# Kernel tuning notes

Measured on AMD Instinct MI355X. Metric: run time of the kernel, lower is better.

Reference implementation:

```python
import jax, jax.numpy as jnp
import numpy as np

N, M, D = 8192, 8192, 256

def setup_inputs() -> dict:
    key = jax.random.key(0)
    kx, ky = jax.random.split(key)
    x = jax.random.normal(kx, (N, D), dtype=jnp.float32)
    y = jax.random.normal(ky, (M, D), dtype=jnp.float32)
    gamma = jnp.float32(1.0)  # learnable scalar parameter
    return {"x": x, "y": y, "gamma": gamma}

def reference(x, y, gamma):
    # Flatten trailing dims (matches x.view(x.size(0), -1))
    x = x.reshape(x.shape[0], -1)
    y = y.reshape(y.shape[0], -1)
    x_sq = jnp.sum(x * x, axis=-1)  # [N]
    y_sq = jnp.sum(y * y, axis=-1)  # [M]
    xy = x @ y.T                    # [N, M]
    sqdist = jnp.maximum(x_sq[:, None] + y_sq[None, :] - 2.0 * xy, 0.0)
    return jnp.exp(-gamma * sqdist)
```

## Files before the change

### kernel.cpp

```cpp
#include <hip/hip_runtime.h>
#include <stdint.h>


typedef __attribute__((ext_vector_type(4))) float f32x4;
typedef __attribute__((ext_vector_type(8))) int   i32x8;

#define NN 8192
#define MM 8192
#define DD 256
#define BK 128

__global__ __launch_bounds__(256) void prep_kernel(
    const float* __restrict__ x, const float* __restrict__ y,
    unsigned char* __restrict__ xb, unsigned char* __restrict__ yb,
    float* __restrict__ xsq, float* __restrict__ ysq) {
  const int lane = threadIdx.x & 63;
  const int row  = blockIdx.x * 4 + (threadIdx.x >> 6);

  const float* src = x;
  unsigned char* dst = xb;
  float* sq = xsq;
  int r = row;
  if (row >= NN) { src = y; dst = yb; sq = ysq; r = row - NN; }

  const float4 v = reinterpret_cast<const float4*>(src + (size_t)r * DD)[lane];
  float s = v.x * v.x + v.y * v.y + v.z * v.z + v.w * v.w;

  int w = 0;
  w = __builtin_amdgcn_cvt_pk_fp8_f32(v.x, v.y, w, false);
  w = __builtin_amdgcn_cvt_pk_fp8_f32(v.z, v.w, w, true);
  reinterpret_cast<int*>(dst + (size_t)r * DD)[lane] = w;

  #pragma unroll
  for (int o = 32; o > 0; o >>= 1) s += __shfl_down(s, o);
  if (lane == 0) sq[r] = s;
}

__global__ __launch_bounds__(256, 2) void rbf_gemm_kernel(
    const unsigned char* __restrict__ xb, const unsigned char* __restrict__ yb,
    const float* __restrict__ xsq, const float* __restrict__ ysq,
    const float* __restrict__ gamma, float* __restrict__ out) {
  __shared__ unsigned char As[128 * BK];
  __shared__ unsigned char Bs[128 * BK];

  const int tid   = threadIdx.x;
  const int lane  = tid & 63;
  const int wave  = tid >> 6;
  const int waveM = wave >> 1;
  const int waveN = wave & 1;
  const int row0  = blockIdx.y * 128;
  const int col0  = blockIdx.x * 128;

  f32x4 acc[4][4] = {};

  const int srow = lane >> 3;
  const int sseg = ((lane & 7) ^ (lane >> 3)) * 16;

  const int fm = lane & 15;
  const int g  = lane >> 4;
  const int off_lo = fm * 128 + (((2 * g)     ^ (fm & 7)) * 16);
  const int off_hi = fm * 128 + (((2 * g + 1) ^ (fm & 7)) * 16);

  #pragma unroll
  for (int kt = 0; kt < 2; ++kt) {
    const int kk = kt * BK;
    __syncthreads();
    #pragma unroll
    for (int q = 0; q < 2; ++q) {
      const int c = wave * 2 + q;
      #pragma unroll
      for (int p = 0; p < 2; ++p) {
        const unsigned char* ga =
            xb + (size_t)(row0 + c * 16 + p * 8 + srow) * DD + kk + sseg;
        __builtin_amdgcn_global_load_lds(
            (const __attribute__((address_space(1))) void*)ga,
            (__attribute__((address_space(3))) void*)(As + c * 2048 + p * 1024),
            16, 0, 0);
        const unsigned char* gb =
            yb + (size_t)(col0 + c * 16 + p * 8 + srow) * DD + kk + sseg;
        __builtin_amdgcn_global_load_lds(
            (const __attribute__((address_space(1))) void*)gb,
            (__attribute__((address_space(3))) void*)(Bs + c * 2048 + p * 1024),
            16, 0, 0);
      }
    }
    __syncthreads();

    i32x8 a[4], b[4];
    #pragma unroll
    for (int i = 0; i < 4; ++i) {
      const unsigned char* base = As + (waveM * 4 + i) * 2048;
      const int4 lo = *reinterpret_cast<const int4*>(base + off_lo);
      const int4 hi = *reinterpret_cast<const int4*>(base + off_hi);
      a[i][0] = lo.x; a[i][1] = lo.y; a[i][2] = lo.z; a[i][3] = lo.w;
      a[i][4] = hi.x; a[i][5] = hi.y; a[i][6] = hi.z; a[i][7] = hi.w;
    }
    #pragma unroll
    for (int j = 0; j < 4; ++j) {
      const unsigned char* base = Bs + (waveN * 4 + j) * 2048;
      const int4 lo = *reinterpret_cast<const int4*>(base + off_lo);
      const int4 hi = *reinterpret_cast<const int4*>(base + off_hi);
      b[j][0] = lo.x; b[j][1] = lo.y; b[j][2] = lo.z; b[j][3] = lo.w;
      b[j][4] = hi.x; b[j][5] = hi.y; b[j][6] = hi.z; b[j][7] = hi.w;
    }

    #pragma unroll
    for (int i = 0; i < 4; ++i)
      #pragma unroll
      for (int j = 0; j < 4; ++j)
        acc[i][j] = __builtin_amdgcn_mfma_scale_f32_16x16x128_f8f6f4(
            a[i], b[j], acc[i][j], 0, 0,
            0, 0x7F7F7F7F, 0, 0x7F7F7F7F);
  }

  const float gm = gamma[0];
  const int colb = col0 + waveN * 64 + (lane & 15);
  float ysv[4];
  #pragma unroll
  for (int j = 0; j < 4; ++j) ysv[j] = ysq[colb + j * 16];

  #pragma unroll
  for (int i = 0; i < 4; ++i) {
    #pragma unroll
    for (int r = 0; r < 4; ++r) {
      const int row = row0 + waveM * 64 + i * 16 + (lane >> 4) * 4 + r;
      const float xsv = xsq[row];
      #pragma unroll
      for (int j = 0; j < 4; ++j) {
        float s = xsv + ysv[j] - 2.0f * acc[i][j][r];
        s = fmaxf(s, 0.0f);
        __builtin_nontemporal_store(__expf(-gm * s),
                                    out + (size_t)row * MM + colb + j * 16);
      }
    }
  }
}

extern "C" void kernel_launch(void* const* d_in, const int* in_sizes, int n_in,
                              void* d_out, int out_size, void* d_ws, size_t ws_size,
                              hipStream_t stream) {
  const float* x     = (const float*)d_in[0];
  const float* y     = (const float*)d_in[1];
  const float* gamma = (const float*)d_in[2];
  float* out = (float*)d_out;

  unsigned char* xb = (unsigned char*)d_ws;
  unsigned char* yb = xb + (size_t)NN * DD;
  float* xsq = (float*)(yb + (size_t)MM * DD);
  float* ysq = xsq + NN;

  prep_kernel<<<(NN + MM) / 4, 256, 0, stream>>>(x, y, xb, yb, xsq, ysq);

  dim3 grid(MM / 128, NN / 128);
  rbf_gemm_kernel<<<grid, 256, 0, stream>>>(xb, yb, xsq, ysq, gamma, out);
}
```

Before: 287.1 us.

## Swap GEMM operand roles for vectorized float4 output stores and wider LDS reads

Swaps the MFMA A/B operands (y tiles into A, x tiles into B), so each lane's four accumulator values now run along output columns and can be written as a single float4 store. It also changes the LDS swizzle so each lane's 32-byte fragment is contiguous, letting one i32x8 load replace two int4 loads. The epilogue loads ysq as float4 and uses plain stores instead of nontemporal scalar stores. The aim is to cut store instruction count and improve write coalescing for the bandwidth-bound 256MB output, at the cost of losing the nontemporal hint and possibly adding LDS bank conflicts under the new swizzle.

```diff
diff --git a/kernel.cpp b/kernel.cpp
--- a/kernel.cpp
+++ b/kernel.cpp
@@ -54,12 +54,12 @@
   f32x4 acc[4][4] = {};
 
   const int srow = lane >> 3;
-  const int sseg = ((lane & 7) ^ (lane >> 3)) * 16;
+  const int spos = lane & 7;
+  const int sseg = ((spos & 1) | (((spos >> 1) ^ (srow & 3)) << 1)) * 16;
 
   const int fm = lane & 15;
   const int g  = lane >> 4;
-  const int off_lo = fm * 128 + (((2 * g)     ^ (fm & 7)) * 16);
-  const int off_hi = fm * 128 + (((2 * g + 1) ^ (fm & 7)) * 16);
+  const int foff = fm * 128 + ((g ^ (fm & 3)) * 32);
 
   #pragma unroll
   for (int kt = 0; kt < 2; ++kt) {
@@ -71,13 +71,13 @@
       #pragma unroll
       for (int p = 0; p < 2; ++p) {
         const unsigned char* ga =
-            xb + (size_t)(row0 + c * 16 + p * 8 + srow) * DD + kk + sseg;
+            yb + (size_t)(col0 + c * 16 + p * 8 + srow) * DD + kk + sseg;
         __builtin_amdgcn_global_load_lds(
             (const __attribute__((address_space(1))) void*)ga,
             (__attribute__((address_space(3))) void*)(As + c * 2048 + p * 1024),
             16, 0, 0);
         const unsigned char* gb =
-            yb + (size_t)(col0 + c * 16 + p * 8 + srow) * DD + kk + sseg;
+            xb + (size_t)(row0 + c * 16 + p * 8 + srow) * DD + kk + sseg;
         __builtin_amdgcn_global_load_lds(
             (const __attribute__((address_space(1))) void*)gb,
             (__attribute__((address_space(3))) void*)(Bs + c * 2048 + p * 1024),
@@ -88,21 +88,11 @@
 
     i32x8 a[4], b[4];
     #pragma unroll
-    for (int i = 0; i < 4; ++i) {
-      const unsigned char* base = As + (waveM * 4 + i) * 2048;
-      const int4 lo = *reinterpret_cast<const int4*>(base + off_lo);
-      const int4 hi = *reinterpret_cast<const int4*>(base + off_hi);
-      a[i][0] = lo.x; a[i][1] = lo.y; a[i][2] = lo.z; a[i][3] = lo.w;
-      a[i][4] = hi.x; a[i][5] = hi.y; a[i][6] = hi.z; a[i][7] = hi.w;
-    }
+    for (int i = 0; i < 4; ++i)
+      a[i] = *reinterpret_cast<const i32x8*>(As + (waveM * 4 + i) * 2048 + foff);
     #pragma unroll
-    for (int j = 0; j < 4; ++j) {
-      const unsigned char* base = Bs + (waveN * 4 + j) * 2048;
-      const int4 lo = *reinterpret_cast<const int4*>(base + off_lo);
-      const int4 hi = *reinterpret_cast<const int4*>(base + off_hi);
-      b[j][0] = lo.x; b[j][1] = lo.y; b[j][2] = lo.z; b[j][3] = lo.w;
-      b[j][4] = hi.x; b[j][5] = hi.y; b[j][6] = hi.z; b[j][7] = hi.w;
-    }
+    for (int j = 0; j < 4; ++j)
+      b[j] = *reinterpret_cast<const i32x8*>(Bs + (waveN * 4 + j) * 2048 + foff);
 
     #pragma unroll
     for (int i = 0; i < 4; ++i)
@@ -114,24 +104,29 @@
   }
 
   const float gm = gamma[0];
-  const int colb = col0 + waveN * 64 + (lane & 15);
-  float ysv[4];
+  const int rowb = row0 + waveN * 64 + (lane & 15);
+  const int colq = col0 + waveM * 64 + (lane >> 4) * 4;
+
+  float xsv[4];
   #pragma unroll
-  for (int j = 0; j < 4; ++j) ysv[j] = ysq[colb + j * 16];
+  for (int j = 0; j < 4; ++j) xsv[j] = xsq[rowb + j * 16];
+  float4 ysv[4];
+  #pragma unroll
+  for (int i = 0; i < 4; ++i)
+    ysv[i] = *reinterpret_cast<const float4*>(ysq + colq + i * 16);
 
   #pragma unroll
-  for (int i = 0; i < 4; ++i) {
+  for (int j = 0; j < 4; ++j) {
+    const size_t obase = (size_t)(rowb + j * 16) * MM;
     #pragma unroll
-    for (int r = 0; r < 4; ++r) {
-      const int row = row0 + waveM * 64 + i * 16 + (lane >> 4) * 4 + r;
-      const float xsv = xsq[row];
-      #pragma unroll
-      for (int j = 0; j < 4; ++j) {
-        float s = xsv + ysv[j] - 2.0f * acc[i][j][r];
-        s = fmaxf(s, 0.0f);
-        __builtin_nontemporal_store(__expf(-gm * s),
-                                    out + (size_t)row * MM + colb + j * 16);
-      }
+    for (int i = 0; i < 4; ++i) {
+      float4 v;
+      float s;
+      s = xsv[j] + ysv[i].x - 2.0f * acc[i][j][0]; v.x = __expf(-gm * fmaxf(s, 0.0f));
+      s = xsv[j] + ysv[i].y - 2.0f * acc[i][j][1]; v.y = __expf(-gm * fmaxf(s, 0.0f));
+      s = xsv[j] + ysv[i].z - 2.0f * acc[i][j][2]; v.z = __expf(-gm * fmaxf(s, 0.0f));
+      s = xsv[j] + ysv[i].w - 2.0f * acc[i][j][3]; v.w = __expf(-gm * fmaxf(s, 0.0f));
+      *reinterpret_cast<float4*>(out + obase + colq + i * 16) = v;
     }
   }
 }
```

After: 284.0 us. No clear change (-1.1%).
